# Performance work log

Hardware: AMD Instinct MI355X
Metric: run time of the kernel (lower is better)

Reference implementation:

```python
import jax, jax.numpy as jnp
import numpy as np

D_MODEL = 2048
N_HEADS = 32
N_KVHEADS = 8
HEAD_DIM = D_MODEL // N_HEADS  # 64
N_GROUPS = N_HEADS // N_KVHEADS  # 4
B, L = 2, 2048


def setup_inputs() -> dict:
    key = jax.random.key(0)
    k1, k2, k3 = jax.random.split(key, 3)
    x = jax.random.normal(k1, (B, L, D_MODEL), dtype=jnp.float32)
    W_qkv = jax.random.normal(k2, (D_MODEL, HEAD_DIM * (N_HEADS + 2 * N_KVHEADS)), dtype=jnp.float32) * 0.02
    W_out = jax.random.normal(k3, (D_MODEL, D_MODEL), dtype=jnp.float32) * 0.02
    # additive causal mask, broadcasts over (b, g, h, l, j)
    neg = jnp.float32(-1e9)
    mask = jnp.where(jnp.tril(jnp.ones((L, L), dtype=bool)), jnp.float32(0.0), neg)
    return {"x": x, "mask": mask, "W_qkv": W_qkv, "W_out": W_out}


def reference(x, mask, W_qkv, W_out):
    b, l, _ = x.shape
    qkv = x @ W_qkv  # (b, l, hd*(H + 2*KVH))
    q, k, v = jnp.split(qkv, [N_HEADS * HEAD_DIM, (N_HEADS + N_KVHEADS) * HEAD_DIM], axis=-1)
    # NOTE: faithful to the original: plain row-major reshapes (no seq/head transpose)
    q = q.reshape(b, N_GROUPS, N_KVHEADS, l, HEAD_DIM)  # (b, g, h, l, d)
    k = k.reshape(b, N_KVHEADS, l, HEAD_DIM)            # (b, h, j, d)
    v = v.reshape(b, N_KVHEADS, l, HEAD_DIM)            # (b, h, j, d)
    scores = jnp.einsum('bghld,bhjd->bghlj', q, k) * (HEAD_DIM ** -0.5)
    scores = scores + mask  # mask broadcasts over leading dims
    attn = jax.nn.softmax(scores, axis=-1)
    out = jnp.einsum('bghlj,bhjd->bghld', attn, v)  # (b, g, h, l, d)
    # rearrange 'b g h l d -> b l (g h d)'
    out = jnp.transpose(out, (0, 3, 1, 2, 4)).reshape(b, l, D_MODEL)
    return out @ W_out
```

## Files before the change

### kernel.cpp

```cpp
#include <hip/hip_runtime.h>
#include <stdint.h>


typedef unsigned short u16;
typedef unsigned int u32;
typedef __attribute__((ext_vector_type(8))) short bf16x8;
typedef __attribute__((ext_vector_type(4))) float f32x4;

__device__ __forceinline__ u16 f2bf(float f) {
  union { float f; uint32_t u; } v; v.f = f;
  uint32_t u = v.u;
  u += 0x7fffu + ((u >> 16) & 1u);
  return (u16)(u >> 16);
}

__device__ __forceinline__ f32x4 mfma16(bf16x8 a, bf16x8 b, f32x4 c) {
  return __builtin_amdgcn_mfma_f32_16x16x32_bf16(a, b, c, 0, 0, 0);
}

__device__ __forceinline__ uint32_t cvt_pk_bf16(float a, float b) {
  uint32_t r;
  asm("v_cvt_pk_bf16_f32 %0, %1, %2" : "=v"(r) : "v"(a), "v"(b));
  return r;
}

__device__ __forceinline__ float fmax3(float a, float b, float c) {
  float d;
  asm("v_max3_f32 %0, %1, %2, %3" : "=v"(d) : "v"(a), "v"(b), "v"(c));
  return d;
}

__device__ __forceinline__ float exp2fast(float x) {
  return __builtin_amdgcn_exp2f(x);
}

__device__ __forceinline__ void gload16(const u16* g, u16* l) {
  __builtin_amdgcn_global_load_lds((__attribute__((address_space(1))) void*)g,
                                   (__attribute__((address_space(3))) void*)l, 16, 0, 0);
}

__global__ __launch_bounds__(256) void cvt_f32_bf16(const float* __restrict__ in,
                                                    u16* __restrict__ out, int n4) {
  int i = blockIdx.x * blockDim.x + threadIdx.x;
  if (i < n4) {
    float4 v = ((const float4*)in)[i];
    uint2 o;
    o.x = (uint32_t)f2bf(v.x) | ((uint32_t)f2bf(v.y) << 16);
    o.y = (uint32_t)f2bf(v.z) | ((uint32_t)f2bf(v.w) << 16);
    ((uint2*)out)[i] = o;
  }
}

__global__ __launch_bounds__(256) void transpose_cvt(const float* __restrict__ in,
                                                     u16* __restrict__ out, int R, int C) {
  __shared__ float tile[32][33];
  int c0 = blockIdx.x * 32, r0 = blockIdx.y * 32;
  int tx = threadIdx.x, ty = threadIdx.y;
#pragma unroll
  for (int k = 0; k < 32; k += 8)
    tile[ty + k][tx] = in[(size_t)(r0 + ty + k) * C + c0 + tx];
  __syncthreads();
#pragma unroll
  for (int k = 0; k < 32; k += 8)
    out[(size_t)(c0 + ty + k) * R + r0 + tx] = f2bf(tile[tx][ty + k]);
}

template <bool OUTF32>
__global__ __launch_bounds__(256) void gemm_bf16(const u16* __restrict__ A,
                                                 const u16* __restrict__ Bt,
                                                 void* __restrict__ C,
                                                 int M, int N, int K) {
  __shared__ __align__(16) u16 As[128 * 32];
  __shared__ __align__(16) u16 Bs[128 * 32];
  int tid = threadIdx.x;
  int lane = tid & 63, w = tid >> 6;
  int wm = (w >> 1) * 64, wn = (w & 1) * 64;

  int nwg = gridDim.x * gridDim.y;
  int lin = blockIdx.y * gridDim.x + blockIdx.x;
  int lin2 = (lin & 7) * (nwg >> 3) + (lin >> 3);
  int bxs = lin2 % gridDim.x, bys = lin2 / gridDim.x;
  int bm = bys * 128, bn = bxs * 128;

  int c = lane & 15, g = lane >> 4;

  const int srow = w * 16 + (lane >> 2);
  const int scol = (lane & 3) * 8;
  const u16* aP = A + (size_t)(bm + srow) * K + scol;
  const u16* bP = Bt + (size_t)(bn + srow) * K + scol;
  const size_t rowskip = (size_t)64 * K;
  u16* aL0 = &As[(w * 16) * 32];
  u16* aL1 = &As[(64 + w * 16) * 32];
  u16* bL0 = &Bs[(w * 16) * 32];
  u16* bL1 = &Bs[(64 + w * 16) * 32];

  f32x4 zero = {0.f, 0.f, 0.f, 0.f};
  f32x4 acc[4][4];
#pragma unroll
  for (int mi = 0; mi < 4; mi++)
#pragma unroll
    for (int ni = 0; ni < 4; ni++) acc[mi][ni] = zero;

  for (int kt = 0; kt < K; kt += 32) {
    gload16(aP + kt, aL0);
    gload16(aP + kt + rowskip, aL1);
    gload16(bP + kt, bL0);
    gload16(bP + kt + rowskip, bL1);
    __syncthreads();
    bf16x8 af[4], bfr[4];
#pragma unroll
    for (int i = 0; i < 4; i++) af[i] = *(const bf16x8*)&As[(wm + i * 16 + c) * 32 + g * 8];
#pragma unroll
    for (int i = 0; i < 4; i++) bfr[i] = *(const bf16x8*)&Bs[(wn + i * 16 + c) * 32 + g * 8];
#pragma unroll
    for (int mi = 0; mi < 4; mi++)
#pragma unroll
      for (int ni = 0; ni < 4; ni++)
        acc[mi][ni] = mfma16(af[mi], bfr[ni], acc[mi][ni]);
    __syncthreads();
  }

#pragma unroll
  for (int mi = 0; mi < 4; mi++)
#pragma unroll
    for (int ni = 0; ni < 4; ni++)
#pragma unroll
      for (int i = 0; i < 4; i++) {
        int row = bm + wm + mi * 16 + g * 4 + i;
        int col = bn + wn + ni * 16 + c;
        float v = acc[mi][ni][i];
        if (OUTF32)
          ((float*)C)[(size_t)row * N + col] = v;
        else
          ((u16*)C)[(size_t)row * N + col] = f2bf(v);
      }
}

__global__ __launch_bounds__(256, 2) void attn_fwd(const u16* __restrict__ qkv,
                                                   u16* __restrict__ attn) {
  __shared__ __align__(16) u16 Ks[2][64][72];
  __shared__ __align__(16) u16 Vs[2][64][72];
  __shared__ __align__(16) u16 Ps[4][32][64];
  const int tid = threadIdx.x;
  const int lane = tid & 63, w = tid >> 6;
  const int c = lane & 15, g = lane >> 4;
  const float C2 = 0.18033688011112042f;

  const int bid = blockIdx.x;
  const int slot = bid >> 3;
  const int head = (bid & 7) * 8 + (slot >> 3);
  const int p = slot & 7;
  const int qtA = p, qtB = 15 - p;
  const int b = head >> 5, gh = head & 31, h = gh & 7;
  const u16* qb = qkv + (size_t)b * 6291456;
  const int qbaseA = qtA * 128 + w * 32;
  const int qbaseB = qtB * 128 + w * 32;

  const u16* qrowA = qb + (size_t)(gh * 64 + qtA * 4 + w) * 3072;
  const u16* qrowB = qb + (size_t)(gh * 64 + qtB * 4 + w) * 3072;
  bf16x8 qfA[2][2], qfB[2][2];
#pragma unroll
  for (int qs = 0; qs < 2; qs++)
#pragma unroll
    for (int kd = 0; kd < 2; kd++) {
      qfA[qs][kd] = *(const bf16x8*)(qrowA + (qs * 16 + c) * 64 + kd * 32 + g * 8);
      qfB[qs][kd] = *(const bf16x8*)(qrowB + (qs * 16 + c) * 64 + kd * 32 + g * 8);
    }

  const f32x4 zero = {0.f, 0.f, 0.f, 0.f};
  f32x4 oA[2][4], oB[2][4];
#pragma unroll
  for (int qs = 0; qs < 2; qs++)
#pragma unroll
    for (int dt = 0; dt < 4; dt++) { oA[qs][dt] = zero; oB[qs][dt] = zero; }
  float mA[2] = {-1e30f, -1e30f}, sA[2] = {0.f, 0.f};
  float mB[2] = {-1e30f, -1e30f}, sB[2] = {0.f, 0.f};

  const int kj = tid >> 2, kd16 = (tid & 3) * 16;
  const int vj0 = (tid >> 4) * 4, vd = (tid & 15) * 4;
  const int vsw = (tid & 7) << 3;
  uint4 kreg0, kreg1;
  uint2 vreg[4];

  auto LOAD = [&](int t) {
    int j = t * 64 + kj;
    const u16* kr = qb + (size_t)(h * 256 + (j >> 3)) * 3072 + 2048 + (j & 7) * 64;
    kreg0 = *(const uint4*)(kr + kd16);
    kreg1 = *(const uint4*)(kr + kd16 + 8);
#pragma unroll
    for (int r = 0; r < 4; r++) {
      int jv = t * 64 + vj0 + r;
      const u16* vr = qb + (size_t)(h * 256 + (jv >> 3)) * 3072 + 2560 + (jv & 7) * 64;
      vreg[r] = *(const uint2*)(vr + vd);
    }
  };
  auto EX = [](uint2 v, int e) -> uint32_t {
    uint32_t x = (e < 2) ? v.x : v.y;
    return (e & 1) ? (x >> 16) : (x & 0xffffu);
  };
  auto STORE = [&](int buf) {
    *(uint4*)&Ks[buf][kj][kd16] = kreg0;
    *(uint4*)&Ks[buf][kj][kd16 + 8] = kreg1;
#pragma unroll
    for (int e = 0; e < 4; e++) {
      uint2 wv;
      wv.x = EX(vreg[0], e) | (EX(vreg[1], e) << 16);
      wv.y = EX(vreg[2], e) | (EX(vreg[3], e) << 16);
      *(uint2*)&Vs[buf][vd + e][vj0 ^ vsw] = wv;
    }
  };

  auto computeQ = [&](int t, int qbase, bf16x8 (&qf)[2][2], bf16x8 (&kf)[4][2],
                      f32x4 (&o)[2][4], float (&m_i)[2], float (&s_i)[2], int cur) {
    const bool diag = (t * 64 + 63 > qbase);
#pragma unroll
    for (int qs = 0; qs < 2; qs++) {
      f32x4 sc[4];
      __builtin_amdgcn_s_setprio(1);
#pragma unroll
      for (int kvt = 0; kvt < 4; kvt++) {
        f32x4 s = mfma16(kf[kvt][0], qf[qs][0], zero);
        sc[kvt] = mfma16(kf[kvt][1], qf[qs][1], s);
      }
      __builtin_amdgcn_s_setprio(0);
      const int q = qbase + qs * 16 + c;
      if (diag) {
#pragma unroll
        for (int kvt = 0; kvt < 4; kvt++)
#pragma unroll
          for (int i = 0; i < 4; i++)
            if (t * 64 + kvt * 16 + g * 4 + i > q) sc[kvt][i] = -1e30f;
      }
      float tmax = fmax3(sc[0][0], sc[0][1], sc[0][2]);
      tmax = fmax3(tmax, sc[0][3], sc[1][0]);
      tmax = fmax3(tmax, sc[1][1], sc[1][2]);
      tmax = fmax3(tmax, sc[1][3], sc[2][0]);
      tmax = fmax3(tmax, sc[2][1], sc[2][2]);
      tmax = fmax3(tmax, sc[2][3], sc[3][0]);
      tmax = fmax3(tmax, sc[3][1], sc[3][2]);
      tmax = fmaxf(tmax, sc[3][3]);
      tmax = fmaxf(tmax, __shfl_xor(tmax, 16));
      tmax = fmaxf(tmax, __shfl_xor(tmax, 32));
      if (!__all(tmax <= m_i[qs] + 64.0f)) {
        float mn = fmaxf(m_i[qs], tmax);
        float corr = exp2fast((m_i[qs] - mn) * C2);
        m_i[qs] = mn;
        s_i[qs] *= corr;
#pragma unroll
        for (int i = 0; i < 4; i++) {
          float cb = __shfl(corr, g * 4 + i);
#pragma unroll
          for (int dt = 0; dt < 4; dt++) o[qs][dt][i] *= cb;
        }
      }
      const float nmc = -m_i[qs] * C2;
      float rs = 0.f;
#pragma unroll
      for (int kvt = 0; kvt < 4; kvt++)
#pragma unroll
        for (int i = 0; i < 4; i++) {
          float pv = exp2fast(fmaf(sc[kvt][i], C2, nmc));
          sc[kvt][i] = pv;
          rs += pv;
        }
      rs += __shfl_xor(rs, 16);
      rs += __shfl_xor(rs, 32);
      s_i[qs] += rs;
      const int pr = qs * 16 + c;
      const int sw = (c & 7) << 3;
#pragma unroll
      for (int kvt = 0; kvt < 4; kvt++) {
        uint2 pw;
        pw.x = cvt_pk_bf16(sc[kvt][0], sc[kvt][1]);
        pw.y = cvt_pk_bf16(sc[kvt][2], sc[kvt][3]);
        *(uint2*)&Ps[w][pr][(kvt * 16 + g * 4) ^ sw] = pw;
      }
    }
    __builtin_amdgcn_s_setprio(1);
#pragma unroll
    for (int kt2 = 0; kt2 < 2; kt2++) {
      bf16x8 bv[4];
#pragma unroll
      for (int dt = 0; dt < 4; dt++) {
        const int vr = dt * 16 + c;
        const int sv = ((dt * 4 + (c >> 2)) & 7) << 3;
        bv[dt] = *(const bf16x8*)&Vs[cur][vr][(kt2 * 32 + g * 8) ^ sv];
      }
#pragma unroll
      for (int qs = 0; qs < 2; qs++) {
        const int pr = qs * 16 + c;
        bf16x8 pa = *(const bf16x8*)&Ps[w][pr][(kt2 * 32 + g * 8) ^ ((c & 7) << 3)];
#pragma unroll
        for (int dt = 0; dt < 4; dt++) o[qs][dt] = mfma16(pa, bv[dt], o[qs][dt]);
      }
    }
    __builtin_amdgcn_s_setprio(0);
  };

  const int nt = 2 * qtB + 2;
  const int jtA = (qbaseA + 31) >> 6;
  const int jtB = (qbaseB + 31) >> 6;

  LOAD(0);
  STORE(0);
  __syncthreads();

  for (int t = 0; t < nt; ++t) {
    const int cur = t & 1;
    if (t + 1 < nt) LOAD(t + 1);
    if (t <= jtB) {
      bf16x8 kf[4][2];
#pragma unroll
      for (int kvt = 0; kvt < 4; kvt++)
#pragma unroll
        for (int kd = 0; kd < 2; kd++)
          kf[kvt][kd] = *(const bf16x8*)&Ks[cur][kvt * 16 + c][kd * 32 + g * 8];
      if (t <= jtA) computeQ(t, qbaseA, qfA, kf, oA, mA, sA, cur);
      computeQ(t, qbaseB, qfB, kf, oB, mB, sB, cur);
    }
    if (t + 1 < nt) STORE(cur ^ 1);
    __syncthreads();
  }

  auto epi = [&](int qbase, f32x4 (&o)[2][4], float (&s_i)[2]) {
#pragma unroll
    for (int qs = 0; qs < 2; qs++)
#pragma unroll
      for (int i = 0; i < 4; i++) {
        float sd = __shfl(s_i[qs], g * 4 + i);
        float inv = 1.0f / sd;
        int row = qbase + qs * 16 + g * 4 + i;
        u16* orow = attn + ((size_t)(b * 2048 + row)) * 2048 + gh * 64;
#pragma unroll
        for (int dt = 0; dt < 4; dt++) orow[dt * 16 + c] = f2bf(o[qs][dt][i] * inv);
      }
  };
  epi(qbaseA, oA, sA);
  epi(qbaseB, oB, sB);
}

extern "C" void kernel_launch(void* const* d_in, const int* in_sizes, int n_in,
                              void* d_out, int out_size, void* d_ws, size_t ws_size,
                              hipStream_t stream) {
  const float* x = (const float*)d_in[0];
  const float* Wqkv = (const float*)d_in[2];
  const float* Wout = (const float*)d_in[3];
  float* out = (float*)d_out;

  u16* xb = (u16*)d_ws;
  u16* wqkvT = xb + 8388608;
  u16* woutT = wqkvT + 6291456;
  u16* qkv = woutT + 4194304;
  u16* attn = qkv + 12582912;

  cvt_f32_bf16<<<8192, 256, 0, stream>>>(x, xb, 2097152);
  transpose_cvt<<<dim3(3072 / 32, 2048 / 32), dim3(32, 8), 0, stream>>>(Wqkv, wqkvT, 2048, 3072);
  transpose_cvt<<<dim3(2048 / 32, 2048 / 32), dim3(32, 8), 0, stream>>>(Wout, woutT, 2048, 2048);
  gemm_bf16<false><<<dim3(3072 / 128, 4096 / 128), 256, 0, stream>>>(xb, wqkvT, qkv, 4096, 3072, 2048);
  attn_fwd<<<512, 256, 0, stream>>>(qkv, attn);
  gemm_bf16<true><<<dim3(2048 / 128, 4096 / 128), 256, 0, stream>>>(attn, woutT, out, 4096, 2048, 2048);
}
```

Baseline: 211.6 us.

## Double-buffer GEMM LDS tiles and XOR-swizzle columns to avoid bank conflicts

Turns the bf16 GEMM main loop into a two-stage pipeline: the global-to-LDS load for the next K tile is issued into the alternate buffer while MFMAs consume the current one, with one barrier per iteration. It also XOR-swizzles the 16-byte column chunk on both the load side and the fragment-read side to reduce LDS bank conflicts. LDS use per block doubles, which may lower occupancy. Correctness depends on the swizzle matching between writer and reader lanes and on the barrier placement.

```diff
diff --git a/kernel.cpp b/kernel.cpp
--- a/kernel.cpp
+++ b/kernel.cpp
@@ -70,8 +70,8 @@
                                                  const u16* __restrict__ Bt,
                                                  void* __restrict__ C,
                                                  int M, int N, int K) {
-  __shared__ __align__(16) u16 As[128 * 32];
-  __shared__ __align__(16) u16 Bs[128 * 32];
+  __shared__ __align__(16) u16 As[2][128 * 32];
+  __shared__ __align__(16) u16 Bs[2][128 * 32];
   int tid = threadIdx.x;
   int lane = tid & 63, w = tid >> 6;
   int wm = (w >> 1) * 64, wn = (w & 1) * 64;
@@ -85,14 +85,10 @@
   int c = lane & 15, g = lane >> 4;
 
   const int srow = w * 16 + (lane >> 2);
-  const int scol = (lane & 3) * 8;
+  const int scol = (((lane & 3) ^ ((lane >> 3) & 3))) * 8;
   const u16* aP = A + (size_t)(bm + srow) * K + scol;
   const u16* bP = Bt + (size_t)(bn + srow) * K + scol;
   const size_t rowskip = (size_t)64 * K;
-  u16* aL0 = &As[(w * 16) * 32];
-  u16* aL1 = &As[(64 + w * 16) * 32];
-  u16* bL0 = &Bs[(w * 16) * 32];
-  u16* bL1 = &Bs[(64 + w * 16) * 32];
 
   f32x4 zero = {0.f, 0.f, 0.f, 0.f};
   f32x4 acc[4][4];
@@ -101,17 +97,29 @@
 #pragma unroll
     for (int ni = 0; ni < 4; ni++) acc[mi][ni] = zero;
 
-  for (int kt = 0; kt < K; kt += 32) {
-    gload16(aP + kt, aL0);
-    gload16(aP + kt + rowskip, aL1);
-    gload16(bP + kt, bL0);
-    gload16(bP + kt + rowskip, bL1);
-    __syncthreads();
+  auto STAGE = [&](int kt, int buf) {
+    u16* aL = &As[buf][(w * 16) * 32];
+    u16* bL = &Bs[buf][(w * 16) * 32];
+    gload16(aP + kt, aL);
+    gload16(aP + kt + rowskip, aL + 64 * 32);
+    gload16(bP + kt, bL);
+    gload16(bP + kt + rowskip, bL + 64 * 32);
+  };
+
+  const int nk = K >> 5;
+  STAGE(0, 0);
+  __syncthreads();
+
+  const int fq = (g ^ ((c >> 1) & 3)) * 8;
+
+  for (int t = 0; t < nk; ++t) {
+    const int cur = t & 1;
+    if (t + 1 < nk) STAGE((t + 1) << 5, cur ^ 1);
     bf16x8 af[4], bfr[4];
 #pragma unroll
-    for (int i = 0; i < 4; i++) af[i] = *(const bf16x8*)&As[(wm + i * 16 + c) * 32 + g * 8];
-#pragma unroll
-    for (int i = 0; i < 4; i++) bfr[i] = *(const bf16x8*)&Bs[(wn + i * 16 + c) * 32 + g * 8];
+    for (int i = 0; i < 4; i++) af[i] = *(const bf16x8*)&As[cur][(wm + i * 16 + c) * 32 + fq];
+#pragma unroll
+    for (int i = 0; i < 4; i++) bfr[i] = *(const bf16x8*)&Bs[cur][(wn + i * 16 + c) * 32 + fq];
 #pragma unroll
     for (int mi = 0; mi < 4; mi++)
 #pragma unroll
```

Measured after the change: 195.8 us. 7.5% less time.
